# Performance work log

Measured on AMD Instinct MI355X. Metric: run time of the kernel, lower is better.

Reference implementation:

```python
import jax, jax.numpy as jnp
import numpy as np

NUM_HEADS = 16
NUM_EXPERTS = 8
TOP_K = 2
LN_EPS = 1e-5


def _layernorm(x, g, b):
    mu = x.mean(-1, keepdims=True)
    var = ((x - mu) ** 2).mean(-1, keepdims=True)
    return (x - mu) * jax.lax.rsqrt(var + LN_EPS) * g + b


def _rope(x, cos, sin):
    # x: [B,S,H,D]; cos/sin: [S, D//2]; interleaved even/odd pairs
    B, S, H, D = x.shape
    xr = x.reshape(B, S, H, D // 2, 2)
    xe, xo = xr[..., 0], xr[..., 1]
    c = cos[None, :, None, :]
    s = sin[None, :, None, :]
    ye = xe * c - xo * s
    yo = xe * s + xo * c
    return jnp.stack((ye, yo), axis=-1).reshape(B, S, H, D)


def setup_inputs() -> dict:
    key = jax.random.key(0)
    ks = jax.random.split(key, 8)
    B, S, D = 4, 512, 1024
    E, Hd = NUM_EXPERTS, 1792
    sc = 0.02
    return {
        'x': jax.random.normal(ks[0], (B, S, D), jnp.float32),
        'ln1_g': jnp.ones((D,), jnp.float32),
        'ln1_b': jnp.zeros((D,), jnp.float32),
        'ln2_g': jnp.ones((D,), jnp.float32),
        'ln2_b': jnp.zeros((D,), jnp.float32),
        'w_qkv': jax.random.normal(ks[1], (D, 3 * D), jnp.float32) * sc,
        'w_o': jax.random.normal(ks[2], (D, D), jnp.float32) * sc,
        'gate_w': jax.random.normal(ks[3], (D, E), jnp.float32) * sc,
        'w_gate': jax.random.normal(ks[4], (E, D, Hd), jnp.float32) * sc,
        'w_up': jax.random.normal(ks[5], (E, D, Hd), jnp.float32) * sc,
        'w_down': jax.random.normal(ks[6], (E, Hd, D), jnp.float32) * sc,
    }


def reference(x, ln1_g, ln1_b, ln2_g, ln2_b, w_qkv, w_o, gate_w, w_gate, w_up, w_down):
    B, S, D = x.shape
    H = NUM_HEADS
    hd = D // H

    # --- attention with RoPE ---
    xn = _layernorm(x, ln1_g, ln1_b)
    qkv = xn @ w_qkv                      # [B,S,3D]
    q, k, v = jnp.split(qkv, 3, axis=-1)
    q = q.reshape(B, S, H, hd)
    k = k.reshape(B, S, H, hd)
    v = v.reshape(B, S, H, hd)
    inv_freq = 1.0 / (10000.0 ** (jnp.arange(0, hd, 2, dtype=jnp.float32) / hd))
    t = jnp.arange(S, dtype=jnp.float32)
    freqs = jnp.outer(t, inv_freq)        # [S, hd//2]
    cos, sin = jnp.cos(freqs), jnp.sin(freqs)
    q = _rope(q, cos, sin)
    k = _rope(k, cos, sin)
    scale = 1.0 / jnp.sqrt(jnp.asarray(hd, x.dtype))
    scores = jnp.einsum('bshd,bthd->bhst', q, k) * scale
    causal = jnp.tril(jnp.ones((S, S), bool))
    scores = jnp.where(causal[None, None], scores, jnp.finfo(scores.dtype).min)
    attn = jax.nn.softmax(scores, axis=-1)
    attn_out = jnp.einsum('bhst,bthd->bshd', attn, v).reshape(B, S, D)
    x = x + attn_out @ w_o

    # --- MoE ---
    xn2 = _layernorm(x, ln2_g, ln2_b)
    xf = xn2.reshape(-1, D)               # [T, D]
    logits = (xf.astype(jnp.bfloat16) @ gate_w.astype(jnp.bfloat16)).astype(jnp.float32)
    topk_w, topk_i = jax.lax.top_k(logits, TOP_K)
    topk_w = jax.nn.softmax(topk_w, axis=-1)
    probs = jax.nn.softmax(logits, axis=-1)
    expert_dist = probs.mean(0)
    lb_loss = NUM_EXPERTS * (expert_dist ** 2).sum()
    # dense dispatch: combine weights [T,E], zero where not selected (same math as sort/gather/scatter)
    cw = (jax.nn.one_hot(topk_i, NUM_EXPERTS, dtype=xf.dtype) * topk_w[..., None].astype(xf.dtype)).sum(1)
    g = jnp.einsum('td,edh->teh', xf, w_gate)
    u = jnp.einsum('td,edh->teh', xf, w_up)
    h = jax.nn.silu(g) * u
    down = jnp.einsum('teh,ehd->ted', h, w_down)
    moe_out = jnp.einsum('ted,te->td', down, cw).reshape(B, S, D)
    x = x + moe_out
    return (x, lb_loss, expert_dist)
```

## Files before the change

kernel.cpp:

```cpp
#include <hip/hip_runtime.h>
#include <hip/hip_bf16.h>
#include <math.h>

#define B_    4
#define S_    512
#define D_    1024
#define T_    2048
#define H_    16
#define HD_   64
#define E_    8
#define HID_  1792
#define D3_   3072
#define GU_   (2 * HID_)

typedef unsigned short ushort_t;
typedef __bf16 bf16x8 __attribute__((ext_vector_type(8)));
typedef float  floatx4 __attribute__((ext_vector_type(4)));

__device__ inline float bf2f(ushort_t u) {
    return __uint_as_float(((unsigned)u) << 16);
}
__device__ inline ushort_t f2bf(float f) {
    __hip_bfloat16 h = __float2bfloat16(f);
    return __builtin_bit_cast(ushort_t, h);
}

__device__ __forceinline__ void gl2lds16(const ushort_t* g, ushort_t* l) {
    __builtin_amdgcn_global_load_lds(
        (const __attribute__((address_space(1))) void*)g,
        (__attribute__((address_space(3))) void*)l, 16, 0, 0);
}

__global__ __launch_bounds__(256) void transpose_bf16_kernel(
    const float* __restrict__ in, ushort_t* __restrict__ out,
    int R, int C, int mul, int add, long outEstride)
{
    __shared__ float tile[32][33];
    const int bx = blockIdx.x * 32;
    const int by = blockIdx.y * 32;
    const size_t iofs = (size_t)blockIdx.z * R * C;
    const size_t oofs = (size_t)blockIdx.z * outEstride;
    const int tx = threadIdx.x & 31;
    const int ty = threadIdx.x >> 5;
#pragma unroll
    for (int i = 0; i < 4; i++) {
        int r = by + ty + i * 8;
        tile[ty + i * 8][tx] = in[iofs + (size_t)r * C + bx + tx];
    }
    __syncthreads();
#pragma unroll
    for (int i = 0; i < 4; i++) {
        int c = bx + ty + i * 8;
        out[oofs + (size_t)(c * mul + add) * R + by + tx] = f2bf(tile[tx][ty + i * 8]);
    }
}

__global__ __launch_bounds__(256) void ln_kernel(
    const float* __restrict__ x, const float* __restrict__ g,
    const float* __restrict__ b, float* __restrict__ outf,
    ushort_t* __restrict__ outb)
{
    const int t = blockIdx.x;
    const int tid = threadIdx.x;
    const int wave = tid >> 6, lane = tid & 63;
    const float4 v = ((const float4*)(x + (size_t)t * D_))[tid];

    float s = v.x + v.y + v.z + v.w;
#pragma unroll
    for (int off = 32; off; off >>= 1) s += __shfl_xor(s, off);
    __shared__ float red1[4];
    __shared__ float red2[4];
    if (lane == 0) red1[wave] = s;
    __syncthreads();
    const float mu = (red1[0] + red1[1] + red1[2] + red1[3]) * (1.0f / D_);

    const float dx = v.x - mu, dy = v.y - mu, dz = v.z - mu, dw = v.w - mu;
    float vs = dx * dx + dy * dy + dz * dz + dw * dw;
#pragma unroll
    for (int off = 32; off; off >>= 1) vs += __shfl_xor(vs, off);
    if (lane == 0) red2[wave] = vs;
    __syncthreads();
    const float var = (red2[0] + red2[1] + red2[2] + red2[3]) * (1.0f / D_);
    const float rs = 1.0f / sqrtf(var + 1e-5f);

    const float4 gg = ((const float4*)g)[tid];
    const float4 bb = ((const float4*)b)[tid];
    float4 o;
    o.x = dx * rs * gg.x + bb.x;
    o.y = dy * rs * gg.y + bb.y;
    o.z = dz * rs * gg.z + bb.z;
    o.w = dw * rs * gg.w + bb.w;
    if (outf) ((float4*)(outf + (size_t)t * D_))[tid] = o;
    if (outb) {
        ushort4 ob;
        ob.x = f2bf(o.x); ob.y = f2bf(o.y); ob.z = f2bf(o.z); ob.w = f2bf(o.w);
        ((ushort4*)(outb + (size_t)t * D_))[tid] = ob;
    }
}

template<int TM>
__global__ __launch_bounds__(256) void sgemm_kernel(
    const float* __restrict__ A, const float* __restrict__ B,
    const float* __restrict__ res, float* __restrict__ C,
    float* __restrict__ C2, int M, int N, int K)
{
    constexpr int RM  = TM / 16;
    constexpr int TPR = 256 / TM;
    constexpr int KF  = 16 / TPR;
    __shared__ float As[16][TM + 4];
    __shared__ float Bs[16][68];
    const int tid = threadIdx.x;
    const int m0 = blockIdx.y * TM, n0 = blockIdx.x * 64;
    const int tx = tid & 15, ty = tid >> 4;

    float acc[RM][4] = {};

    const int arow = tid / TPR;
    const int akk  = (tid % TPR) * KF;
    const int bk = tid >> 4;
    const int bc = (tid & 15) * 4;

    const float* Ap = A + (size_t)(m0 + arow) * K + akk;
    const float* Bp = B + (size_t)bk * N + n0 + bc;

    for (int k0 = 0; k0 < K; k0 += 16) {
        float av[KF];
#pragma unroll
        for (int f = 0; f < KF / 4; f++) {
            const float4 t = *(const float4*)(Ap + k0 + f * 4);
            av[f * 4 + 0] = t.x; av[f * 4 + 1] = t.y;
            av[f * 4 + 2] = t.z; av[f * 4 + 3] = t.w;
        }
        const float4 bv = *(const float4*)(Bp + (size_t)k0 * N);
        __syncthreads();
#pragma unroll
        for (int i = 0; i < KF; i++) As[akk + i][arow] = av[i];
        *(float4*)&Bs[bk][bc] = bv;
        __syncthreads();
#pragma unroll
        for (int k = 0; k < 16; k++) {
            float a[RM];
#pragma unroll
            for (int f = 0; f < RM / 4; f++) {
                const float4 t = *(const float4*)&As[k][ty * RM + f * 4];
                a[f * 4 + 0] = t.x; a[f * 4 + 1] = t.y;
                a[f * 4 + 2] = t.z; a[f * 4 + 3] = t.w;
            }
            const float4 bb = *(const float4*)&Bs[k][tx * 4];
            const float bj[4] = {bb.x, bb.y, bb.z, bb.w};
#pragma unroll
            for (int i = 0; i < RM; i++)
#pragma unroll
                for (int j = 0; j < 4; j++)
                    acc[i][j] = fmaf(a[i], bj[j], acc[i][j]);
        }
    }

#pragma unroll
    for (int i = 0; i < RM; i++) {
        const int row = m0 + ty * RM + i;
        const size_t base = (size_t)row * N + n0 + tx * 4;
        float4 o;
        o.x = acc[i][0]; o.y = acc[i][1]; o.z = acc[i][2]; o.w = acc[i][3];
        if (res) {
            const float4 r0 = *(const float4*)(res + base);
            o.x += r0.x; o.y += r0.y; o.z += r0.z; o.w += r0.w;
        }
        *(float4*)(C + base) = o;
        if (C2) *(float4*)(C2 + base) = o;
    }
}

__global__ __launch_bounds__(256) void gateup_idx_kernel(
    const ushort_t* __restrict__ A, const ushort_t* __restrict__ Bgu,
    const int* __restrict__ cnt, const int* __restrict__ tok,
    ushort_t* __restrict__ Hc)
{
    const int e = blockIdx.z;
    const int cntE = cnt[e];
    const int row0 = blockIdx.y * 128;
    if (row0 >= cntE) return;
    const int col0 = blockIdx.x * 128;
    const ushort_t* Bt = Bgu + (size_t)e * GU_ * D_;
    ushort_t* Hp = Hc + (size_t)e * T_ * HID_;

    __shared__ __align__(16) ushort_t As[128 * 32];
    __shared__ __align__(16) ushort_t Bs[128 * 32];
    const int tid = threadIdx.x, w = tid >> 6, lane = tid & 63;
    const int lr = lane >> 2, lc = (lane & 3) * 8;
    const int wm = (w >> 1) * 64, wn = (w & 1) * 64;
    const int lm = lane & 15, lq = lane >> 4;

    floatx4 acc[4][4] = {};

    int r0c = row0 + w * 16 + lr;  if (r0c > cntE - 1) r0c = cntE - 1;
    int r1c = row0 + 64 + w * 16 + lr; if (r1c > cntE - 1) r1c = cntE - 1;
    const ushort_t* Ap0 = A + (size_t)tok[e * T_ + r0c] * D_ + lc;
    const ushort_t* Ap1 = A + (size_t)tok[e * T_ + r1c] * D_ + lc;
    const ushort_t* Bp = Bt + (size_t)(col0 + w * 16 + lr) * D_ + lc;
    ushort_t* lA = As + w * 512;
    ushort_t* lB = Bs + w * 512;

    for (int k0 = 0; k0 < D_; k0 += 32) {
        __syncthreads();
        gl2lds16(Ap0 + k0, lA);
        gl2lds16(Ap1 + k0, lA + 2048);
        gl2lds16(Bp + k0, lB);
        gl2lds16(Bp + k0 + (size_t)64 * D_, lB + 2048);
        __syncthreads();
        bf16x8 a[4], b[4];
#pragma unroll
        for (int i = 0; i < 4; i++)
            a[i] = *(const bf16x8*)(As + (wm + i * 16 + lm) * 32 + lq * 8);
#pragma unroll
        for (int j = 0; j < 4; j++)
            b[j] = *(const bf16x8*)(Bs + (wn + j * 16 + lm) * 32 + lq * 8);
#pragma unroll
        for (int i = 0; i < 4; i++)
#pragma unroll
            for (int j = 0; j < 4; j++)
                acc[i][j] = __builtin_amdgcn_mfma_f32_16x16x32_bf16(a[i], b[j], acc[i][j], 0, 0, 0);
    }

#pragma unroll
    for (int i = 0; i < 4; i++)
#pragma unroll
        for (int j = 0; j < 4; j++)
#pragma unroll
            for (int r = 0; r < 4; r++) {
                const float v = acc[i][j][r];
                const float vp = __shfl_xor(v, 1);
                const float g = (lm & 1) ? vp : v;
                const float u = (lm & 1) ? v : vp;
                const float h = g / (1.f + __expf(-g)) * u;
                if (!(lm & 1)) {
                    const int row = row0 + wm + i * 16 + lq * 4 + r;
                    const int col = col0 + wn + j * 16 + lm;
                    Hp[(size_t)row * HID_ + (col >> 1)] = f2bf(h);
                }
            }
}

__global__ __launch_bounds__(256) void down_idx_kernel(
    const ushort_t* __restrict__ Hc, const ushort_t* __restrict__ Wd,
    const int* __restrict__ cnt, const int* __restrict__ tok,
    const float* __restrict__ wt, float* __restrict__ out)
{
    const int e = blockIdx.z;
    const int cntE = cnt[e];
    const int row0 = blockIdx.y * 128;
    if (row0 >= cntE) return;
    const int col0 = blockIdx.x * 128;
    const ushort_t* A = Hc + (size_t)e * T_ * HID_;
    const ushort_t* Bt = Wd + (size_t)e * D_ * HID_;

    __shared__ __align__(16) ushort_t As[128 * 32];
    __shared__ __align__(16) ushort_t Bs[128 * 32];
    const int tid = threadIdx.x, w = tid >> 6, lane = tid & 63;
    const int lr = lane >> 2, lc = (lane & 3) * 8;
    const int wm = (w >> 1) * 64, wn = (w & 1) * 64;
    const int lm = lane & 15, lq = lane >> 4;

    floatx4 acc[4][4] = {};

    const ushort_t* Ap = A + (size_t)(row0 + w * 16 + lr) * HID_ + lc;
    const ushort_t* Bp = Bt + (size_t)(col0 + w * 16 + lr) * HID_ + lc;
    ushort_t* lA = As + w * 512;
    ushort_t* lB = Bs + w * 512;

    for (int k0 = 0; k0 < HID_; k0 += 32) {
        __syncthreads();
        gl2lds16(Ap + k0, lA);
        gl2lds16(Ap + k0 + (size_t)64 * HID_, lA + 2048);
        gl2lds16(Bp + k0, lB);
        gl2lds16(Bp + k0 + (size_t)64 * HID_, lB + 2048);
        __syncthreads();
        bf16x8 a[4], b[4];
#pragma unroll
        for (int i = 0; i < 4; i++)
            a[i] = *(const bf16x8*)(As + (wm + i * 16 + lm) * 32 + lq * 8);
#pragma unroll
        for (int j = 0; j < 4; j++)
            b[j] = *(const bf16x8*)(Bs + (wn + j * 16 + lm) * 32 + lq * 8);
#pragma unroll
        for (int i = 0; i < 4; i++)
#pragma unroll
            for (int j = 0; j < 4; j++)
                acc[i][j] = __builtin_amdgcn_mfma_f32_16x16x32_bf16(a[i], b[j], acc[i][j], 0, 0, 0);
    }

#pragma unroll
    for (int i = 0; i < 4; i++)
#pragma unroll
        for (int r = 0; r < 4; r++) {
            const int row = row0 + wm + i * 16 + lq * 4 + r;
            if (row < cntE) {
                const int t = tok[e * T_ + row];
                const float scale = wt[e * T_ + row];
#pragma unroll
                for (int j = 0; j < 4; j++) {
                    const int col = col0 + wn + j * 16 + lm;
                    atomicAdd(&out[(size_t)t * D_ + col], scale * acc[i][j][r]);
                }
            }
        }
}

__global__ __launch_bounds__(256) void rope_table_kernel(
    float* __restrict__ ctab, float* __restrict__ stab)
{
    const int i = blockIdx.x * 256 + threadIdx.x;
    if (i >= S_ * 32) return;
    const int s = i >> 5, p = i & 31;
    const double e = (double)(2 * p) / 64.0;
    const float pf = (float)pow(10000.0, e);
    const float invf = 1.0f / pf;
    const float fr = (float)s * invf;
    ctab[i] = (float)cos((double)fr);
    stab[i] = (float)sin((double)fr);
}

__global__ __launch_bounds__(256) void rope_kernel(
    float* __restrict__ qkv, const float* __restrict__ ctab,
    const float* __restrict__ stab)
{
    const int n = blockIdx.x * 256 + threadIdx.x;
    const int pair = n & 31;
    const int h = (n >> 5) & 15;
    const int t = n >> 9;
    const int s = t & (S_ - 1);
    const float c = ctab[s * 32 + pair];
    const float sn = stab[s * 32 + pair];
    const size_t base = (size_t)t * D3_ + h * HD_ + pair * 2;
    float x0 = qkv[base], x1 = qkv[base + 1];
    qkv[base]     = x0 * c - x1 * sn;
    qkv[base + 1] = x0 * sn + x1 * c;
    x0 = qkv[base + D_]; x1 = qkv[base + D_ + 1];
    qkv[base + D_]     = x0 * c - x1 * sn;
    qkv[base + D_ + 1] = x0 * sn + x1 * c;
}

__global__ __launch_bounds__(256) void attn_kernel(
    const float* __restrict__ qkv, float* __restrict__ out)
{
    __shared__ __align__(16) float kbuf[64][68];
    __shared__ float vbuf[64][65];
    __shared__ __align__(16) float qs[32][64];
    __shared__ __align__(16) float ps[4][8][64];

    const int b = blockIdx.z, h = blockIdx.y;
    const int qt = (int)gridDim.x - 1 - (int)blockIdx.x;
    const int tid = threadIdx.x, wave = tid >> 6, lane = tid & 63;
    const int q0 = qt * 32;

    for (int i = tid; i < 32 * 64; i += 256) {
        const int qi = i >> 6, d = i & 63;
        const int t = b * S_ + q0 + qi;
        qs[qi][d] = qkv[(size_t)t * D3_ + h * HD_ + d];
    }

    float m[8], l[8], O[8];
#pragma unroll
    for (int qi = 0; qi < 8; qi++) { m[qi] = -INFINITY; l[qi] = 0.f; O[qi] = 0.f; }

    const int maxS = q0 + 31;
    for (int c0 = 0; c0 <= maxS; c0 += 64) {
        __syncthreads();
        for (int i = tid; i < 64 * 16; i += 256) {
            const int key = i >> 4, g = i & 15;
            const int t = b * S_ + c0 + key;
            const float4 kv = *(const float4*)(qkv + (size_t)t * D3_ + D_ + h * HD_ + g * 4);
            const float4 vv = *(const float4*)(qkv + (size_t)t * D3_ + 2 * D_ + h * HD_ + g * 4);
            *(float4*)&kbuf[key][g * 4] = kv;
            vbuf[key][g * 4 + 0] = vv.x; vbuf[key][g * 4 + 1] = vv.y;
            vbuf[key][g * 4 + 2] = vv.z; vbuf[key][g * 4 + 3] = vv.w;
        }
        __syncthreads();

        const int kglob = c0 + lane;
        float sc[8];
#pragma unroll
        for (int qi = 0; qi < 8; qi++) sc[qi] = 0.f;
#pragma unroll 4
        for (int g = 0; g < 16; g++) {
            const float4 kv = *(const float4*)&kbuf[lane][g * 4];
#pragma unroll
            for (int qi = 0; qi < 8; qi++) {
                const float4 qv = *(const float4*)&qs[wave * 8 + qi][g * 4];
                float s = sc[qi];
                s = fmaf(qv.x, kv.x, s);
                s = fmaf(qv.y, kv.y, s);
                s = fmaf(qv.z, kv.z, s);
                s = fmaf(qv.w, kv.w, s);
                sc[qi] = s;
            }
        }
#pragma unroll
        for (int qi = 0; qi < 8; qi++) {
            const int s = q0 + wave * 8 + qi;
            float v = (kglob <= s) ? sc[qi] * 0.125f : -INFINITY;
            float cmax = v;
#pragma unroll
            for (int off = 32; off; off >>= 1) cmax = fmaxf(cmax, __shfl_xor(cmax, off));
            const float mnew = fmaxf(m[qi], cmax);
            const float alpha = expf(m[qi] - mnew);
            const float p = (v == -INFINITY) ? 0.f : expf(v - mnew);
            float psum = p;
#pragma unroll
            for (int off = 32; off; off >>= 1) psum += __shfl_xor(psum, off);
            l[qi] = l[qi] * alpha + psum;
            m[qi] = mnew;
            ps[wave][qi][lane] = p;
            sc[qi] = alpha;
        }
#pragma unroll
        for (int qi = 0; qi < 8; qi++) O[qi] *= sc[qi];
#pragma unroll 4
        for (int g = 0; g < 16; g++) {
            const float v0 = vbuf[g * 4 + 0][lane];
            const float v1 = vbuf[g * 4 + 1][lane];
            const float v2 = vbuf[g * 4 + 2][lane];
            const float v3 = vbuf[g * 4 + 3][lane];
#pragma unroll
            for (int qi = 0; qi < 8; qi++) {
                const float4 p4 = *(const float4*)&ps[wave][qi][g * 4];
                float o = O[qi];
                o = fmaf(p4.x, v0, o);
                o = fmaf(p4.y, v1, o);
                o = fmaf(p4.z, v2, o);
                o = fmaf(p4.w, v3, o);
                O[qi] = o;
            }
        }
    }

#pragma unroll
    for (int qi = 0; qi < 8; qi++) {
        const int t = b * S_ + q0 + wave * 8 + qi;
        out[(size_t)t * D_ + h * HD_ + lane] = O[qi] / l[qi];
    }
}

__global__ __launch_bounds__(64) void gate_kernel(
    const ushort_t* __restrict__ xn2, const float* __restrict__ gate_w,
    int* __restrict__ cnt, int* __restrict__ tok, float* __restrict__ wt,
    float* __restrict__ probs)
{
    const int t = blockIdx.x;
    const int lane = threadIdx.x;
    float acc[8] = {0, 0, 0, 0, 0, 0, 0, 0};
    for (int d = lane; d < D_; d += 64) {
        const float xv = bf2f(xn2[(size_t)t * D_ + d]);
        const float4 g0 = ((const float4*)(gate_w + d * 8))[0];
        const float4 g1 = ((const float4*)(gate_w + d * 8))[1];
        acc[0] = fmaf(xv, bf2f(f2bf(g0.x)), acc[0]);
        acc[1] = fmaf(xv, bf2f(f2bf(g0.y)), acc[1]);
        acc[2] = fmaf(xv, bf2f(f2bf(g0.z)), acc[2]);
        acc[3] = fmaf(xv, bf2f(f2bf(g0.w)), acc[3]);
        acc[4] = fmaf(xv, bf2f(f2bf(g1.x)), acc[4]);
        acc[5] = fmaf(xv, bf2f(f2bf(g1.y)), acc[5]);
        acc[6] = fmaf(xv, bf2f(f2bf(g1.z)), acc[6]);
        acc[7] = fmaf(xv, bf2f(f2bf(g1.w)), acc[7]);
    }
#pragma unroll
    for (int e = 0; e < 8; e++) {
#pragma unroll
        for (int off = 32; off; off >>= 1) acc[e] += __shfl_xor(acc[e], off);
        acc[e] = bf2f(f2bf(acc[e]));
    }

    if (lane == 0) {
        int i1 = 0;
        for (int e = 1; e < 8; e++) if (acc[e] > acc[i1]) i1 = e;
        int i2 = (i1 == 0) ? 1 : 0;
        for (int e = 0; e < 8; e++) if (e != i1 && acc[e] > acc[i2]) i2 = e;
        const float e2 = expf(acc[i2] - acc[i1]);
        const float w1 = 1.f / (1.f + e2);
        const float w2 = e2 * w1;
        const int p1 = atomicAdd(&cnt[i1], 1);
        tok[i1 * T_ + p1] = t; wt[i1 * T_ + p1] = w1;
        const int p2 = atomicAdd(&cnt[i2], 1);
        tok[i2 * T_ + p2] = t; wt[i2 * T_ + p2] = w2;
        const float mx = acc[i1];
        float se = 0.f, pe[8];
        for (int e = 0; e < 8; e++) { pe[e] = expf(acc[e] - mx); se += pe[e]; }
        const float inv = 1.f / se;
        for (int e = 0; e < 8; e++) probs[t * 8 + e] = pe[e] * inv;
    }
}

__global__ void zero_route_kernel(int* __restrict__ cnt)
{
    if (threadIdx.x < 8) cnt[threadIdx.x] = 0;
}

__global__ __launch_bounds__(256) void reduce_dist_kernel(
    const float* __restrict__ probs, float* __restrict__ out)
{
    __shared__ float part[256];
    __shared__ float dist8[8];
    const int tid = threadIdx.x;
    const int e = tid & 7, chunk = tid >> 3;
    float s = 0.f;
    for (int t = chunk; t < T_; t += 32) s += probs[t * 8 + e];
    part[tid] = s;
    __syncthreads();
    if (tid < 8) {
        float tot = 0.f;
        for (int c = 0; c < 32; c++) tot += part[c * 8 + tid];
        const float dv = tot * (1.0f / T_);
        dist8[tid] = dv;
        out[(size_t)T_ * D_ + 1 + tid] = dv;
    }
    __syncthreads();
    if (tid == 0) {
        float s2 = 0.f;
        for (int k = 0; k < 8; k++) s2 += dist8[k] * dist8[k];
        out[(size_t)T_ * D_] = (float)E_ * s2;
    }
}

extern "C" void kernel_launch(void* const* d_in, const int* in_sizes, int n_in,
                              void* d_out, int out_size, void* d_ws, size_t ws_size,
                              hipStream_t stream)
{
    const float* x      = (const float*)d_in[0];
    const float* ln1_g  = (const float*)d_in[1];
    const float* ln1_b  = (const float*)d_in[2];
    const float* ln2_g  = (const float*)d_in[3];
    const float* ln2_b  = (const float*)d_in[4];
    const float* w_qkv  = (const float*)d_in[5];
    const float* w_o    = (const float*)d_in[6];
    const float* gate_w = (const float*)d_in[7];
    const float* w_gate = (const float*)d_in[8];
    const float* w_up   = (const float*)d_in[9];
    const float* w_down = (const float*)d_in[10];
    float* out = (float*)d_out;

    char* ws = (char*)d_ws;
    size_t off = 0;
    auto alloc = [&](size_t bytes) { size_t o = off; off += (bytes + 255) & ~(size_t)255; return o; };
    ushort_t* wguT  = (ushort_t*)(ws + alloc((size_t)E_ * GU_ * D_ * 2));
    ushort_t* wdT   = (ushort_t*)(ws + alloc((size_t)E_ * D_ * HID_ * 2));
    float*    xn    = (float*)   (ws + alloc((size_t)T_ * D_ * 4));
    ushort_t* xn2   = (ushort_t*)(ws + alloc((size_t)T_ * D_ * 2));
    int*      cnt   = (int*)     (ws + alloc(64));
    int*      tok   = (int*)     (ws + alloc((size_t)E_ * T_ * 4));
    float*    wt    = (float*)   (ws + alloc((size_t)E_ * T_ * 4));
    float*    probs = (float*)   (ws + alloc((size_t)T_ * E_ * 4));
    float*    ctab  = (float*)   (ws + alloc((size_t)S_ * 32 * 4));
    float*    stab  = (float*)   (ws + alloc((size_t)S_ * 32 * 4));
    const size_t scratch0 = alloc((size_t)E_ * T_ * HID_ * 2);
    float*    qkv   = (float*)   (ws + scratch0);
    float*    attnO = (float*)   (ws + scratch0 + (size_t)T_ * D3_ * 4);
    float*    x1    = (float*)   (ws + scratch0 + (size_t)T_ * D3_ * 4 + (size_t)T_ * D_ * 4);
    ushort_t* Hc    = (ushort_t*)(ws + scratch0);
    (void)ws_size; (void)in_sizes; (void)n_in; (void)out_size;

    hipLaunchKernelGGL(transpose_bf16_kernel, dim3(HID_ / 32, D_ / 32, E_), dim3(256), 0, stream,
                       w_gate, wguT, D_, HID_, 2, 0, (long)GU_ * D_);
    hipLaunchKernelGGL(transpose_bf16_kernel, dim3(HID_ / 32, D_ / 32, E_), dim3(256), 0, stream,
                       w_up, wguT, D_, HID_, 2, 1, (long)GU_ * D_);
    hipLaunchKernelGGL(transpose_bf16_kernel, dim3(D_ / 32, HID_ / 32, E_), dim3(256), 0, stream,
                       w_down, wdT, HID_, D_, 1, 0, (long)D_ * HID_);

    hipLaunchKernelGGL(rope_table_kernel, dim3((S_ * 32 + 255) / 256), dim3(256), 0, stream,
                       ctab, stab);

    hipLaunchKernelGGL(ln_kernel, dim3(T_), dim3(256), 0, stream,
                       x, ln1_g, ln1_b, xn, (ushort_t*)nullptr);

    hipLaunchKernelGGL((sgemm_kernel<128>), dim3(D3_ / 64, T_ / 128), dim3(256), 0, stream,
                       xn, w_qkv, (const float*)nullptr, qkv, (float*)nullptr, T_, D3_, D_);

    hipLaunchKernelGGL(rope_kernel, dim3(T_ * H_ * 32 / 256), dim3(256), 0, stream,
                       qkv, ctab, stab);

    hipLaunchKernelGGL(attn_kernel, dim3(S_ / 32, H_, B_), dim3(256), 0, stream, qkv, attnO);

    hipLaunchKernelGGL((sgemm_kernel<64>), dim3(D_ / 64, T_ / 64), dim3(256), 0, stream,
                       attnO, w_o, x, x1, out, T_, D_, D_);

    hipLaunchKernelGGL(ln_kernel, dim3(T_), dim3(256), 0, stream,
                       x1, ln2_g, ln2_b, (float*)nullptr, xn2);

    hipLaunchKernelGGL(zero_route_kernel, dim3(1), dim3(64), 0, stream, cnt);
    hipLaunchKernelGGL(gate_kernel, dim3(T_), dim3(64), 0, stream,
                       xn2, gate_w, cnt, tok, wt, probs);
    hipLaunchKernelGGL(reduce_dist_kernel, dim3(1), dim3(256), 0, stream, probs, out);

    hipLaunchKernelGGL(gateup_idx_kernel, dim3(GU_ / 128, T_ / 128, E_), dim3(256), 0, stream,
                       xn2, wguT, cnt, tok, Hc);
    hipLaunchKernelGGL(down_idx_kernel, dim3(D_ / 128, T_ / 128, E_), dim3(256), 0, stream,
                       Hc, wdT, cnt, tok, wt, out);
}
```

Before: 857.3 us.

## Split causal attention over key chunks with a separate softmax-merge kernel

Replaces the single attention kernel, which walked all causal key chunks serially per query tile, with a split-K scheme. Each block now handles one (query tile, key chunk) pair and writes a partial output plus its row max and sum. A second kernel merges the partials using log-sum-exp rescaling. The aim is more parallel blocks and less load imbalance across causal tiles, at the cost of extra global traffic for the partials, a second launch, and a larger, re-aliased workspace.

```diff
diff --git a/kernel.cpp b/kernel.cpp
--- a/kernel.cpp
+++ b/kernel.cpp
@@ -12,10 +12,13 @@
 #define HID_  1792
 #define D3_   3072
 #define GU_   (2 * HID_)
+#define NPART_ 72
 
 typedef unsigned short ushort_t;
 typedef __bf16 bf16x8 __attribute__((ext_vector_type(8)));
 typedef float  floatx4 __attribute__((ext_vector_type(4)));
+
+__constant__ int kPrefix[16] = {0,1,2,4,6,9,12,16,20,25,30,36,42,49,56,64};
 
 __device__ inline float bf2f(ushort_t u) {
     return __uint_as_float(((unsigned)u) << 16);
@@ -340,105 +343,141 @@
     qkv[base + D_ + 1] = x0 * sn + x1 * c;
 }
 
-__global__ __launch_bounds__(256) void attn_kernel(
-    const float* __restrict__ qkv, float* __restrict__ out)
-{
+__global__ __launch_bounds__(256) void attn_part_kernel(
+    const float* __restrict__ qkv, float* __restrict__ Opart,
+    float* __restrict__ Ml)
+{
+    const int qt = blockIdx.y;
+    const int kc = blockIdx.x;
+    if (kc > (qt >> 1)) return;
+    const int bh = blockIdx.z;
+    const int b = bh >> 4, h = bh & 15;
+    const int q0 = qt * 32;
+    const int c0 = kc * 64;
+    const int pidx = bh * NPART_ + kPrefix[qt] + kc;
+
     __shared__ __align__(16) float kbuf[64][68];
-    __shared__ float vbuf[64][65];
-    __shared__ __align__(16) float qs[32][64];
-    __shared__ __align__(16) float ps[4][8][64];
-
-    const int b = blockIdx.z, h = blockIdx.y;
-    const int qt = (int)gridDim.x - 1 - (int)blockIdx.x;
+    __shared__ __align__(16) float vbuf[64][68];
+    __shared__ __align__(16) float qs[32][68];
+    __shared__ __align__(16) float ps[4][8][68];
+
     const int tid = threadIdx.x, wave = tid >> 6, lane = tid & 63;
-    const int q0 = qt * 32;
-
-    for (int i = tid; i < 32 * 64; i += 256) {
-        const int qi = i >> 6, d = i & 63;
+
+    for (int i = tid; i < 32 * 16; i += 256) {
+        const int qi = i >> 4, g = i & 15;
         const int t = b * S_ + q0 + qi;
-        qs[qi][d] = qkv[(size_t)t * D3_ + h * HD_ + d];
-    }
-
-    float m[8], l[8], O[8];
-#pragma unroll
-    for (int qi = 0; qi < 8; qi++) { m[qi] = -INFINITY; l[qi] = 0.f; O[qi] = 0.f; }
-
-    const int maxS = q0 + 31;
-    for (int c0 = 0; c0 <= maxS; c0 += 64) {
-        __syncthreads();
-        for (int i = tid; i < 64 * 16; i += 256) {
-            const int key = i >> 4, g = i & 15;
-            const int t = b * S_ + c0 + key;
-            const float4 kv = *(const float4*)(qkv + (size_t)t * D3_ + D_ + h * HD_ + g * 4);
-            const float4 vv = *(const float4*)(qkv + (size_t)t * D3_ + 2 * D_ + h * HD_ + g * 4);
-            *(float4*)&kbuf[key][g * 4] = kv;
-            vbuf[key][g * 4 + 0] = vv.x; vbuf[key][g * 4 + 1] = vv.y;
-            vbuf[key][g * 4 + 2] = vv.z; vbuf[key][g * 4 + 3] = vv.w;
+        *(float4*)&qs[qi][g * 4] =
+            *(const float4*)(qkv + (size_t)t * D3_ + h * HD_ + g * 4);
+    }
+    for (int i = tid; i < 64 * 16; i += 256) {
+        const int key = i >> 4, g = i & 15;
+        const int t = b * S_ + c0 + key;
+        *(float4*)&kbuf[key][g * 4] =
+            *(const float4*)(qkv + (size_t)t * D3_ + D_ + h * HD_ + g * 4);
+        *(float4*)&vbuf[key][g * 4] =
+            *(const float4*)(qkv + (size_t)t * D3_ + 2 * D_ + h * HD_ + g * 4);
+    }
+    __syncthreads();
+
+    const int kglob = c0 + lane;
+    float sc[8];
+#pragma unroll
+    for (int qi = 0; qi < 8; qi++) sc[qi] = 0.f;
+#pragma unroll 4
+    for (int g = 0; g < 16; g++) {
+        const float4 kv = *(const float4*)&kbuf[lane][g * 4];
+#pragma unroll
+        for (int qi = 0; qi < 8; qi++) {
+            const float4 qv = *(const float4*)&qs[wave * 8 + qi][g * 4];
+            float s = sc[qi];
+            s = fmaf(qv.x, kv.x, s);
+            s = fmaf(qv.y, kv.y, s);
+            s = fmaf(qv.z, kv.z, s);
+            s = fmaf(qv.w, kv.w, s);
+            sc[qi] = s;
         }
-        __syncthreads();
-
-        const int kglob = c0 + lane;
-        float sc[8];
-#pragma unroll
-        for (int qi = 0; qi < 8; qi++) sc[qi] = 0.f;
+    }
+#pragma unroll
+    for (int qi = 0; qi < 8; qi++) {
+        const int s = q0 + wave * 8 + qi;
+        float v = (kglob <= s) ? sc[qi] * 0.125f : -INFINITY;
+        float cmax = v;
+#pragma unroll
+        for (int off = 32; off; off >>= 1) cmax = fmaxf(cmax, __shfl_xor(cmax, off));
+        const float p = (v == -INFINITY) ? 0.f : expf(v - cmax);
+        float psum = p;
+#pragma unroll
+        for (int off = 32; off; off >>= 1) psum += __shfl_xor(psum, off);
+        ps[wave][qi][lane] = p;
+        if (lane == 0) {
+            Ml[(size_t)pidx * 64 + wave * 8 + qi] = cmax;
+            Ml[(size_t)pidx * 64 + 32 + wave * 8 + qi] = psum;
+        }
+    }
+
+    float O[8];
+#pragma unroll
+    for (int qi = 0; qi < 8; qi++) O[qi] = 0.f;
 #pragma unroll 4
-        for (int g = 0; g < 16; g++) {
-            const float4 kv = *(const float4*)&kbuf[lane][g * 4];
-#pragma unroll
-            for (int qi = 0; qi < 8; qi++) {
-                const float4 qv = *(const float4*)&qs[wave * 8 + qi][g * 4];
-                float s = sc[qi];
-                s = fmaf(qv.x, kv.x, s);
-                s = fmaf(qv.y, kv.y, s);
-                s = fmaf(qv.z, kv.z, s);
-                s = fmaf(qv.w, kv.w, s);
-                sc[qi] = s;
-            }
+    for (int g = 0; g < 16; g++) {
+        const float v0 = vbuf[g * 4 + 0][lane];
+        const float v1 = vbuf[g * 4 + 1][lane];
+        const float v2 = vbuf[g * 4 + 2][lane];
+        const float v3 = vbuf[g * 4 + 3][lane];
+#pragma unroll
+        for (int qi = 0; qi < 8; qi++) {
+            const float4 p4 = *(const float4*)&ps[wave][qi][g * 4];
+            float o = O[qi];
+            o = fmaf(p4.x, v0, o);
+            o = fmaf(p4.y, v1, o);
+            o = fmaf(p4.z, v2, o);
+            o = fmaf(p4.w, v3, o);
+            O[qi] = o;
         }
-#pragma unroll
-        for (int qi = 0; qi < 8; qi++) {
-            const int s = q0 + wave * 8 + qi;
-            float v = (kglob <= s) ? sc[qi] * 0.125f : -INFINITY;
-            float cmax = v;
-#pragma unroll
-            for (int off = 32; off; off >>= 1) cmax = fmaxf(cmax, __shfl_xor(cmax, off));
-            const float mnew = fmaxf(m[qi], cmax);
-            const float alpha = expf(m[qi] - mnew);
-            const float p = (v == -INFINITY) ? 0.f : expf(v - mnew);
-            float psum = p;
-#pragma unroll
-            for (int off = 32; off; off >>= 1) psum += __shfl_xor(psum, off);
-            l[qi] = l[qi] * alpha + psum;
-            m[qi] = mnew;
-            ps[wave][qi][lane] = p;
-            sc[qi] = alpha;
-        }
-#pragma unroll
-        for (int qi = 0; qi < 8; qi++) O[qi] *= sc[qi];
-#pragma unroll 4
-        for (int g = 0; g < 16; g++) {
-            const float v0 = vbuf[g * 4 + 0][lane];
-            const float v1 = vbuf[g * 4 + 1][lane];
-            const float v2 = vbuf[g * 4 + 2][lane];
-            const float v3 = vbuf[g * 4 + 3][lane];
-#pragma unroll
-            for (int qi = 0; qi < 8; qi++) {
-                const float4 p4 = *(const float4*)&ps[wave][qi][g * 4];
-                float o = O[qi];
-                o = fmaf(p4.x, v0, o);
-                o = fmaf(p4.y, v1, o);
-                o = fmaf(p4.z, v2, o);
-                o = fmaf(p4.w, v3, o);
-                O[qi] = o;
-            }
-        }
-    }
-
-#pragma unroll
-    for (int qi = 0; qi < 8; qi++) {
-        const int t = b * S_ + q0 + wave * 8 + qi;
-        out[(size_t)t * D_ + h * HD_ + lane] = O[qi] / l[qi];
-    }
+    }
+#pragma unroll
+    for (int qi = 0; qi < 8; qi++)
+        Opart[((size_t)pidx * 32 + wave * 8 + qi) * 64 + lane] = O[qi];
+}
+
+__global__ __launch_bounds__(256) void attn_combine_kernel(
+    const float* __restrict__ Opart, const float* __restrict__ Ml,
+    float* __restrict__ out)
+{
+    const int qt = blockIdx.x, bh = blockIdx.y;
+    const int b = bh >> 4, h = bh & 15;
+    const int nchunk = (qt >> 1) + 1;
+    const int base = bh * NPART_ + kPrefix[qt];
+    const int tid = threadIdx.x;
+    const int qrow = tid >> 3;
+    const int d0 = (tid & 7) * 8;
+
+    float M = -INFINITY;
+    for (int c = 0; c < nchunk; c++)
+        M = fmaxf(M, Ml[(size_t)(base + c) * 64 + qrow]);
+
+    float L = 0.f;
+    float o[8] = {0, 0, 0, 0, 0, 0, 0, 0};
+    for (int c = 0; c < nchunk; c++) {
+        const float mc = Ml[(size_t)(base + c) * 64 + qrow];
+        const float lc = Ml[(size_t)(base + c) * 64 + 32 + qrow];
+        const float w = (mc == -INFINITY) ? 0.f : expf(mc - M);
+        L = fmaf(lc, w, L);
+        const size_t ob = ((size_t)(base + c) * 32 + qrow) * 64 + d0;
+        const float4 a0 = *(const float4*)(Opart + ob);
+        const float4 a1 = *(const float4*)(Opart + ob + 4);
+        o[0] = fmaf(a0.x, w, o[0]); o[1] = fmaf(a0.y, w, o[1]);
+        o[2] = fmaf(a0.z, w, o[2]); o[3] = fmaf(a0.w, w, o[3]);
+        o[4] = fmaf(a1.x, w, o[4]); o[5] = fmaf(a1.y, w, o[5]);
+        o[6] = fmaf(a1.z, w, o[6]); o[7] = fmaf(a1.w, w, o[7]);
+    }
+    const float inv = 1.f / L;
+    const int t = b * S_ + qt * 32 + qrow;
+    float4 r0, r1;
+    r0.x = o[0] * inv; r0.y = o[1] * inv; r0.z = o[2] * inv; r0.w = o[3] * inv;
+    r1.x = o[4] * inv; r1.y = o[5] * inv; r1.z = o[6] * inv; r1.w = o[7] * inv;
+    *(float4*)(out + (size_t)t * D_ + h * HD_ + d0) = r0;
+    *(float4*)(out + (size_t)t * D_ + h * HD_ + d0 + 4) = r1;
 }
 
 __global__ __launch_bounds__(64) void gate_kernel(
@@ -550,10 +589,15 @@
     float*    probs = (float*)   (ws + alloc((size_t)T_ * E_ * 4));
     float*    ctab  = (float*)   (ws + alloc((size_t)S_ * 32 * 4));
     float*    stab  = (float*)   (ws + alloc((size_t)S_ * 32 * 4));
-    const size_t scratch0 = alloc((size_t)E_ * T_ * HID_ * 2);
+    const size_t qkvBytes   = (size_t)T_ * D3_ * 4;
+    const size_t opartBytes = (size_t)64 * NPART_ * 32 * 64 * 4;
+    const size_t mlBytes    = (size_t)64 * NPART_ * 64 * 4;
+    const size_t scratch0 = alloc(qkvBytes + opartBytes + mlBytes);
     float*    qkv   = (float*)   (ws + scratch0);
-    float*    attnO = (float*)   (ws + scratch0 + (size_t)T_ * D3_ * 4);
-    float*    x1    = (float*)   (ws + scratch0 + (size_t)T_ * D3_ * 4 + (size_t)T_ * D_ * 4);
+    float*    Opart = (float*)   (ws + scratch0 + qkvBytes);
+    float*    Ml    = (float*)   (ws + scratch0 + qkvBytes + opartBytes);
+    float*    attnO = (float*)   (ws + scratch0);
+    float*    x1    = (float*)   (ws + scratch0 + (size_t)T_ * D_ * 4);
     ushort_t* Hc    = (ushort_t*)(ws + scratch0);
     (void)ws_size; (void)in_sizes; (void)n_in; (void)out_size;
 
@@ -576,7 +620,10 @@
     hipLaunchKernelGGL(rope_kernel, dim3(T_ * H_ * 32 / 256), dim3(256), 0, stream,
                        qkv, ctab, stab);
 
-    hipLaunchKernelGGL(attn_kernel, dim3(S_ / 32, H_, B_), dim3(256), 0, stream, qkv, attnO);
+    hipLaunchKernelGGL(attn_part_kernel, dim3(8, 16, 64), dim3(256), 0, stream,
+                       qkv, Opart, Ml);
+    hipLaunchKernelGGL(attn_combine_kernel, dim3(16, 64), dim3(256), 0, stream,
+                       Opart, Ml, attnO);
 
     hipLaunchKernelGGL((sgemm_kernel<64>), dim3(D_ / 64, T_ / 64), dim3(256), 0, stream,
                        attnO, w_o, x, x1, out, T_, D_, D_);
```

Result: no change. 841.8 us (-1.8%).
